# Kernel optimization log

Hardware: AMD Instinct MI355X
Metric: run time of the kernel (lower is better)

The kernel has to match this reference:

```python
import jax, jax.numpy as jnp
import numpy as np

L, H, E, V = 8, 16, 1024, 32000   # n_layer, n_head, n_embd, vocab_size
B, T = 4, 1024                      # batch, block_size
HS = E // H                         # head_size = 64


def _ln(x, g, b, eps=1e-5):
    m = jnp.mean(x, axis=-1, keepdims=True)
    v = jnp.mean((x - m) ** 2, axis=-1, keepdims=True)
    return (x - m) / jnp.sqrt(v + eps) * g + b


def setup_inputs() -> dict:
    key = jax.random.key(0)
    ks = jax.random.split(key, 21)
    s = 0.02
    n = lambda k, shp: (jax.random.normal(k, shp, dtype=jnp.float32) * s)
    return {
        'idx': jax.random.randint(ks[0], (B, T), 0, V),
        'tok_emb': n(ks[1], (V, E)),
        'pos_emb': n(ks[2], (T, E)),
        'ln1_g': jnp.ones((L, E), jnp.float32),
        'ln1_b': jnp.zeros((L, E), jnp.float32),
        'Wq': n(ks[3], (L, E, E)),
        'Wk': n(ks[4], (L, E, E)),
        'Wv': n(ks[5], (L, E, E)),
        'Wo': n(ks[6], (L, E, E)),
        'bo': jnp.zeros((L, E), jnp.float32),
        'ln2_g': jnp.ones((L, E), jnp.float32),
        'ln2_b': jnp.zeros((L, E), jnp.float32),
        'W1': n(ks[7], (L, E, 4 * E)),
        'b1': jnp.zeros((L, 4 * E), jnp.float32),
        'W2': n(ks[8], (L, 4 * E, E)),
        'b2': jnp.zeros((L, E), jnp.float32),
        'lnf_g': jnp.ones((E,), jnp.float32),
        'lnf_b': jnp.zeros((E,), jnp.float32),
        'Wlm': n(ks[9], (E, V)),
        'blm': jnp.zeros((V,), jnp.float32),
    }


def reference(idx, tok_emb, pos_emb, ln1_g, ln1_b, Wq, Wk, Wv, Wo, bo,
              ln2_g, ln2_b, W1, b1, W2, b2, lnf_g, lnf_b, Wlm, blm):
    x = tok_emb[idx] + pos_emb[:T]               # [B, T, E]
    scale = E ** -0.5                            # NOTE: source scales by C=n_embd, not head_size
    mask = jnp.tril(jnp.ones((T, T), dtype=bool))
    for l in range(L):
        h = _ln(x, ln1_g[l], ln1_b[l])
        q = (h @ Wq[l]).reshape(B, T, H, HS).transpose(0, 2, 1, 3)   # [B,H,T,hs]
        k = (h @ Wk[l]).reshape(B, T, H, HS).transpose(0, 2, 1, 3)
        v = (h @ Wv[l]).reshape(B, T, H, HS).transpose(0, 2, 1, 3)
        att = jnp.einsum('bhqd,bhkd->bhqk', q, k) * scale
        att = jnp.where(mask, att, -jnp.inf)
        att = jax.nn.softmax(att, axis=-1)
        o = jnp.einsum('bhqk,bhkd->bhqd', att, v)
        o = o.transpose(0, 2, 1, 3).reshape(B, T, E)                 # concat heads
        x = x + o @ Wo[l] + bo[l]
        h2 = _ln(x, ln2_g[l], ln2_b[l])
        x = x + jax.nn.relu(h2 @ W1[l] + b1[l]) @ W2[l] + b2[l]
    x = _ln(x, lnf_g, lnf_b)
    return x @ Wlm + blm                          # logits [B, T, V]
```

## Files before the change

kernel.cpp:

```cpp
#include <hip/hip_runtime.h>
#include <math.h>

#define L_ 8
#define H_ 16
#define E_ 1024
#define V_ 32000
#define B_ 4
#define T_ 1024
#define HS_ 64
#define M_ 4096
#define QKVS_ 3072

typedef __attribute__((ext_vector_type(8))) short short8;
typedef __attribute__((ext_vector_type(4))) float f32x4;

__device__ __forceinline__ unsigned short f2bf(float f) {
  unsigned int u = __builtin_bit_cast(unsigned int, f);
  u += 0x7fffu + ((u >> 16) & 1u);
  return (unsigned short)(u >> 16);
}
__device__ __forceinline__ float bf2f(unsigned short u) {
  unsigned int v = ((unsigned int)u) << 16;
  return __builtin_bit_cast(float, v);
}

__global__ __launch_bounds__(256) void k_embed(
    const int* __restrict__ idx, const float* __restrict__ tok,
    const float* __restrict__ pos, float* __restrict__ x) {
  int bt = blockIdx.x;
  int t  = bt & (T_ - 1);
  int token = idx[bt];
  const float4* te = (const float4*)(tok + (size_t)token * E_);
  const float4* pe = (const float4*)(pos + (size_t)t * E_);
  float4* xo = (float4*)(x + (size_t)bt * E_);
  int i = threadIdx.x;
  float4 a = te[i], b = pe[i];
  xo[i] = make_float4(a.x + b.x, a.y + b.y, a.z + b.z, a.w + b.w);
}

__global__ __launch_bounds__(256) void k_wt(
    const float* __restrict__ W, unsigned short* __restrict__ WT,
    int K, int N, size_t ss, size_t ds) {
  __shared__ unsigned short t[64][66];
  const float* Ws = W + (size_t)blockIdx.z * ss;
  unsigned short* Wd = WT + (size_t)blockIdx.z * ds;
  int n0 = blockIdx.x * 64, k0 = blockIdx.y * 64;
  int tid = threadIdx.x;
  int c = tid & 63, r4 = tid >> 6;
  #pragma unroll
  for (int i = 0; i < 16; ++i) {
    int kr = i * 4 + r4;
    t[kr][c] = f2bf(Ws[(size_t)(k0 + kr) * N + n0 + c]);
  }
  __syncthreads();
  #pragma unroll
  for (int i = 0; i < 16; ++i) {
    int nr = i * 4 + r4;
    Wd[(size_t)(n0 + nr) * K + k0 + c] = t[c][nr];
  }
}

__device__ __forceinline__ float blk_sum256(float v, float* red) {
  #pragma unroll
  for (int o = 1; o < 64; o <<= 1) v += __shfl_xor(v, o);
  int wid = threadIdx.x >> 6, lane = threadIdx.x & 63;
  if (lane == 0) red[wid] = v;
  __syncthreads();
  v = red[0] + red[1] + red[2] + red[3];
  __syncthreads();
  return v;
}

__global__ __launch_bounds__(256) void k_ln_bf(
    const float* __restrict__ X, const float* __restrict__ g,
    const float* __restrict__ b, unsigned short* __restrict__ Y) {
  __shared__ float red[4];
  int row = blockIdx.x;
  int i = threadIdx.x;
  float4 xv = ((const float4*)(X + (size_t)row * E_))[i];
  float s = xv.x + xv.y + xv.z + xv.w;
  s = blk_sum256(s, red);
  float mean = s * (1.0f / E_);
  float dx = xv.x - mean, dy = xv.y - mean, dz = xv.z - mean, dw = xv.w - mean;
  float vs = dx*dx + dy*dy + dz*dz + dw*dw;
  vs = blk_sum256(vs, red);
  float rstd = rsqrtf(vs * (1.0f / E_) + 1e-5f);
  float4 gv = ((const float4*)g)[i];
  float4 bv = ((const float4*)b)[i];
  ushort4 o;
  o.x = f2bf(dx * rstd * gv.x + bv.x);
  o.y = f2bf(dy * rstd * gv.y + bv.y);
  o.z = f2bf(dz * rstd * gv.z + bv.z);
  o.w = f2bf(dw * rstd * gv.w + bv.w);
  ((ushort4*)(Y + (size_t)row * E_))[i] = o;
}

__global__ __launch_bounds__(256) void k_red4ln(
    const unsigned short* __restrict__ p, const float* __restrict__ bias,
    float* __restrict__ xf, const float* __restrict__ g,
    const float* __restrict__ b, unsigned short* __restrict__ hb) {
  __shared__ float red[4];
  const int ME = M_ * E_;
  int row = blockIdx.x;
  int tid = threadIdx.x;
  int i = row * E_ + tid * 4;
  ushort4 a  = *(const ushort4*)(p + i);
  ushort4 b2 = *(const ushort4*)(p + ME + i);
  ushort4 c  = *(const ushort4*)(p + 2 * ME + i);
  ushort4 d  = *(const ushort4*)(p + 3 * ME + i);
  float4 bv = *(const float4*)(bias + tid * 4);
  float4 x  = *(float4*)(xf + i);
  x.x += bf2f(a.x) + bf2f(b2.x) + bf2f(c.x) + bf2f(d.x) + bv.x;
  x.y += bf2f(a.y) + bf2f(b2.y) + bf2f(c.y) + bf2f(d.y) + bv.y;
  x.z += bf2f(a.z) + bf2f(b2.z) + bf2f(c.z) + bf2f(d.z) + bv.z;
  x.w += bf2f(a.w) + bf2f(b2.w) + bf2f(c.w) + bf2f(d.w) + bv.w;
  *(float4*)(xf + i) = x;
  float s = x.x + x.y + x.z + x.w;
  s = blk_sum256(s, red);
  float mean = s * (1.0f / E_);
  float dx = x.x - mean, dy = x.y - mean, dz = x.z - mean, dw = x.w - mean;
  float vs = dx*dx + dy*dy + dz*dz + dw*dw;
  vs = blk_sum256(vs, red);
  float rstd = rsqrtf(vs * (1.0f / E_) + 1e-5f);
  float4 gv = ((const float4*)g)[tid];
  float4 lb = ((const float4*)b)[tid];
  ushort4 o;
  o.x = f2bf(dx * rstd * gv.x + lb.x);
  o.y = f2bf(dy * rstd * gv.y + lb.y);
  o.z = f2bf(dz * rstd * gv.z + lb.z);
  o.w = f2bf(dw * rstd * gv.w + lb.w);
  ((ushort4*)(hb + (size_t)row * E_))[tid] = o;
}

#define GLDS(src, dst) __builtin_amdgcn_global_load_lds( \
    (const __attribute__((address_space(1))) void*)(src), \
    (__attribute__((address_space(3))) void*)(dst), 16, 0, 0)

#define BAR() do { asm volatile("" ::: "memory"); __builtin_amdgcn_s_barrier(); \
                   asm volatile("" ::: "memory"); } while (0)

template<int OT, bool RELU, int DEC, int NF>
__global__ __launch_bounds__(512, 2) void k_gemm_256(
    const unsigned short* __restrict__ A, const unsigned short* __restrict__ BT,
    const float* __restrict__ bias, void* __restrict__ Cout, int N, int K, int Kstr) {
  constexpr int BUFA = 16384;
  constexpr int BUFB = NF * 4096;
  constexpr int BN = NF * 64;
  __shared__ __attribute__((aligned(16))) unsigned short As[2 * BUFA];
  __shared__ __attribute__((aligned(16))) unsigned short Bs[2 * BUFB];
  int tid = threadIdx.x;
  int lane = tid & 63, w = tid >> 6;
  int lr = lane & 15, lq = (lane >> 4) & 3;
  int wm = w >> 2, wn = w & 3;

  int nwg = gridDim.x, orig = blockIdx.x;
  int qq = nwg >> 3, rr = nwg & 7;
  int xcd = orig & 7, lid = orig >> 3;
  int wg = (xcd < rr ? xcd * (qq + 1) : rr * (qq + 1) + (xcd - rr) * qq) + lid;
  int m0, n0, kofs = 0;
  size_t cofs = 0;
  if constexpr (DEC == 0) { m0 = (wg & 15) * 256; n0 = (wg >> 4) * BN; }
  else if constexpr (DEC == 1) {
    int nbn = N / BN;
    int msub = wg & 7;
    int rest = wg >> 3;
    int nb = rest % nbn;
    int msup = rest / nbn;
    m0 = (msup * 8 + msub) * 256;
    n0 = nb * BN;
  } else {
    int inner = wg & 63;
    m0 = (inner & 15) * 256; n0 = (inner >> 4) * BN;
    int ks = wg >> 6;
    kofs = ks * K;
    cofs = (size_t)ks * M_ * (size_t)N;
  }

  int srow = w * 8 + (lane >> 3);
  int skoff = ((lane & 7) ^ (lane >> 3)) * 8;
  const unsigned short* aS = A + (size_t)(m0 + srow) * Kstr + kofs + skoff;
  const unsigned short* bS = BT + (size_t)(n0 + srow) * Kstr + kofs + skoff;

#define STG_A1(bo, g, tt) GLDS(aS + (size_t)((g) * 64) * Kstr + (tt) * 64, \
                               &As[(bo) + (((g) * 64) << 6) + (w << 9)])
#define STG_B1(bo, g, tt) GLDS(bS + (size_t)((g) * 64) * Kstr + (tt) * 64, \
                               &Bs[(bo) + (((g) * 64) << 6) + (w << 9)])
#define LDA_(dst, mh, ks) { _Pragma("unroll") for (int m_ = 0; m_ < 4; ++m_) \
  dst[m_] = *(const short8*)&As[soA + ((wm * 128 + (mh) * 64 + m_ * 16 + lr) << 6) + ((((ks) * 4 + lq) ^ (lr & 7)) << 3)]; }
#define LDB_(dst, ks) { _Pragma("unroll") for (int n_ = 0; n_ < NF; ++n_) \
  dst[n_] = *(const short8*)&Bs[soB + ((wn * (16 * NF) + n_ * 16 + lr) << 6) + ((((ks) * 4 + lq) ^ (lr & 7)) << 3)]; }
#define MMA(afr, mofs) do { __builtin_amdgcn_s_setprio(1); \
  _Pragma("unroll") for (int m_ = 0; m_ < 4; ++m_) { \
    _Pragma("unroll") for (int n_ = 0; n_ < NF; ++n_) \
      acc[(mofs) + m_][n_] = __builtin_amdgcn_mfma_f32_16x16x32_bf16(afr[m_], bfr[n_], acc[(mofs) + m_][n_], 0, 0, 0); } \
  __builtin_amdgcn_s_setprio(0); } while (0)

  f32x4 acc[8][NF] = {};
  const int NT = K >> 6;

  #pragma unroll
  for (int g = 0; g < 4; ++g) STG_A1(0, g, 0);
  #pragma unroll
  for (int g = 0; g < NF; ++g) STG_B1(0, g, 0);
  if (NT > 1) {
    STG_B1(BUFB, 0, 1); STG_B1(BUFB, 1, 1);
    asm volatile("s_waitcnt vmcnt(2)" ::: "memory");
  } else {
    asm volatile("s_waitcnt vmcnt(0)" ::: "memory");
  }
  BAR();

  for (int t = 0; t < NT; ++t) {
    const int soA = (t & 1) * BUFA, soB = (t & 1) * BUFB;
    const int nbA = ((t + 1) & 1) * BUFA, nbB = ((t + 1) & 1) * BUFB;
    short8 af0[4], af1[4], bfr[NF];
    LDA_(af0, 0, 0);
    LDB_(bfr, 0);
    if (t + 1 < NT) {
      STG_B1(nbB, 2, t + 1);
      if constexpr (NF == 4) STG_B1(nbB, 3, t + 1);
    }
    BAR(); MMA(af0, 0); BAR();
    LDA_(af1, 1, 0);
    if (t + 1 < NT) { STG_A1(nbA, 0, t + 1); STG_A1(nbA, 1, t + 1); }
    BAR(); MMA(af1, 4); BAR();
    LDA_(af0, 0, 1);
    LDB_(bfr, 1);
    if (t + 1 < NT) { STG_A1(nbA, 2, t + 1); STG_A1(nbA, 3, t + 1); }
    BAR(); MMA(af0, 0); BAR();
    LDA_(af1, 1, 1);
    if (t + 2 < NT) { STG_B1(soB, 0, t + 2); STG_B1(soB, 1, t + 2); }
    BAR(); MMA(af1, 4);
    if (t + 2 < NT) { asm volatile("s_waitcnt vmcnt(2)" ::: "memory"); }
    else            { asm volatile("s_waitcnt vmcnt(0)" ::: "memory"); }
    BAR();
  }

  #pragma unroll
  for (int m = 0; m < 8; ++m) {
    #pragma unroll
    for (int n = 0; n < NF; ++n) {
      int col = n0 + wn * (16 * NF) + n * 16 + lr;
      float bv = bias ? bias[col] : 0.0f;
      #pragma unroll
      for (int i = 0; i < 4; ++i) {
        size_t row = (size_t)(m0 + wm * 128 + m * 16 + lq * 4 + i);
        float v = acc[m][n][i] + bv;
        if (RELU) v = fmaxf(v, 0.0f);
        if (OT == 0) ((float*)Cout)[cofs + row * N + col] = v;
        else ((unsigned short*)Cout)[cofs + row * N + col] = f2bf(v);
      }
    }
  }
#undef STG_A1
#undef STG_B1
#undef LDA_
#undef LDB_
#undef MMA
}

template<int BN, int OT, bool RELU, bool RES>
__global__ __launch_bounds__(256) void k_gemm_tn(
    const unsigned short* __restrict__ A, const unsigned short* __restrict__ BT,
    const float* __restrict__ bias, const float* __restrict__ R,
    void* __restrict__ Cout, int M, int N, int K) {
  constexpr int NF = BN / 32;
  __shared__ __attribute__((aligned(16))) unsigned short As[128 * 64];
  __shared__ __attribute__((aligned(16))) unsigned short Bs[BN * 64];
  int tid = threadIdx.x;
  int lane = tid & 63, w = tid >> 6;
  int lr = lane & 15, lq = lane >> 4;
  int m0 = blockIdx.x * 128, n0 = blockIdx.y * BN;
  int wr = (w >> 1) * 64, wc = (w & 1) * (BN / 2);

  int srow = w * 8 + (lane >> 3);
  int skoff = ((lane & 7) ^ (lane >> 3)) * 8;
  const unsigned short* a0 = A + (size_t)(m0 + srow) * K + skoff;
  const unsigned short* b0 = BT + (size_t)(n0 + srow) * K + skoff;

  f32x4 acc[4][NF] = {};

  for (int k0 = 0; k0 < K; k0 += 64) {
    __syncthreads();
    #pragma unroll
    for (int j = 0; j < 4; ++j)
      __builtin_amdgcn_global_load_lds(
          (const __attribute__((address_space(1))) void*)(a0 + (size_t)(j * 32) * K + k0),
          (__attribute__((address_space(3))) void*)(As + j * 2048 + w * 512), 16, 0, 0);
    #pragma unroll
    for (int j = 0; j < NF; ++j)
      __builtin_amdgcn_global_load_lds(
          (const __attribute__((address_space(1))) void*)(b0 + (size_t)(j * 32) * K + k0),
          (__attribute__((address_space(3))) void*)(Bs + j * 2048 + w * 512), 16, 0, 0);
    __syncthreads();
    short8 af[4][2], bf[NF][2];
    #pragma unroll
    for (int m = 0; m < 4; ++m)
      #pragma unroll
      for (int ks = 0; ks < 2; ++ks)
        af[m][ks] = *(const short8*)&As[(wr + m * 16 + lr) * 64 + (((ks * 4 + lq) ^ (lr & 7)) << 3)];
    #pragma unroll
    for (int n = 0; n < NF; ++n)
      #pragma unroll
      for (int ks = 0; ks < 2; ++ks)
        bf[n][ks] = *(const short8*)&Bs[(wc + n * 16 + lr) * 64 + (((ks * 4 + lq) ^ (lr & 7)) << 3)];
    #pragma unroll
    for (int ks = 0; ks < 2; ++ks)
      #pragma unroll
      for (int m = 0; m < 4; ++m)
        #pragma unroll
        for (int n = 0; n < NF; ++n)
          acc[m][n] = __builtin_amdgcn_mfma_f32_16x16x32_bf16(af[m][ks], bf[n][ks], acc[m][n], 0, 0, 0);
  }

  #pragma unroll
  for (int m = 0; m < 4; ++m) {
    #pragma unroll
    for (int n = 0; n < NF; ++n) {
      int col = n0 + wc + n * 16 + lr;
      float bv = bias ? bias[col] : 0.0f;
      #pragma unroll
      for (int i = 0; i < 4; ++i) {
        size_t row = (size_t)(m0 + wr + m * 16 + lq * 4 + i);
        float v = acc[m][n][i] + bv;
        if (RELU) v = fmaxf(v, 0.0f);
        if (RES)  v += R[row * N + col];
        if (OT == 0) ((float*)Cout)[row * N + col] = v;
        else ((unsigned short*)Cout)[row * N + col] = f2bf(v);
      }
    }
  }
}

template<int OT, bool RELU, bool RES>
__global__ __launch_bounds__(256) void k_gemm_bf(
    const unsigned short* __restrict__ A, const float* __restrict__ W,
    const float* __restrict__ bias, const float* __restrict__ R,
    void* __restrict__ Cout, int M, int N, int K) {
  __shared__ unsigned short As[128][40];
  __shared__ unsigned short Bs[128][40];
  int tid = threadIdx.x;
  int lane = tid & 63, wid = tid >> 6;
  int m0 = blockIdx.x * 128, n0 = blockIdx.y * 128;
  int wr = (wid >> 1) * 64, wc = (wid & 1) * 64;
  f32x4 acc[4][4] = {};
  int a_row = tid >> 1, a_koff = (tid & 1) * 16;
  int b_nb = tid & 31, b_kb = (tid >> 5) * 4;
  int lr = lane & 15, lq = lane >> 4;
  for (int k0 = 0; k0 < K; k0 += 32) {
    const unsigned short* ap = A + (size_t)(m0 + a_row) * K + k0 + a_koff;
    uint4 av0 = *(const uint4*)ap;
    uint4 av1 = *(const uint4*)(ap + 8);
    float wv[4][4];
    #pragma unroll
    for (int dk = 0; dk < 4; ++dk) {
      const float* wrow = W + (size_t)(k0 + b_kb + dk) * N + n0 + b_nb;
      #pragma unroll
      for (int j = 0; j < 4; ++j) wv[j][dk] = wrow[32 * j];
    }
    __syncthreads();
    *(uint4*)&As[a_row][a_koff]     = av0;
    *(uint4*)&As[a_row][a_koff + 8] = av1;
    #pragma unroll
    for (int j = 0; j < 4; ++j) {
      ushort4 pk;
      pk.x = f2bf(wv[j][0]); pk.y = f2bf(wv[j][1]);
      pk.z = f2bf(wv[j][2]); pk.w = f2bf(wv[j][3]);
      *(ushort4*)&Bs[b_nb + 32 * j][b_kb] = pk;
    }
    __syncthreads();
    short8 af[4], bf[4];
    #pragma unroll
    for (int m = 0; m < 4; ++m) af[m] = *(const short8*)&As[wr + m * 16 + lr][lq * 8];
    #pragma unroll
    for (int n = 0; n < 4; ++n) bf[n] = *(const short8*)&Bs[wc + n * 16 + lr][lq * 8];
    #pragma unroll
    for (int m = 0; m < 4; ++m)
      #pragma unroll
      for (int n = 0; n < 4; ++n)
        acc[m][n] = __builtin_amdgcn_mfma_f32_16x16x32_bf16(af[m], bf[n], acc[m][n], 0, 0, 0);
  }
  #pragma unroll
  for (int m = 0; m < 4; ++m) {
    #pragma unroll
    for (int n = 0; n < 4; ++n) {
      int col = n0 + wc + n * 16 + lr;
      float bv = bias ? bias[col] : 0.0f;
      #pragma unroll
      for (int i = 0; i < 4; ++i) {
        size_t row = (size_t)(m0 + wr + m * 16 + lq * 4 + i);
        float v = acc[m][n][i] + bv;
        if (RELU) v = fmaxf(v, 0.0f);
        if (RES)  v += R[row * N + col];
        if (OT == 0) ((float*)Cout)[row * N + col] = v;
        else ((unsigned short*)Cout)[row * N + col] = f2bf(v);
      }
    }
  }
}

__global__ __launch_bounds__(256) void k_fattn(
    const unsigned short* __restrict__ QKV, unsigned short* __restrict__ O) {
  __shared__ unsigned short Ks[64][72];
  __shared__ unsigned short Vs[64][74];
  __shared__ unsigned short Pl[4][32][72];
  int tid = threadIdx.x;
  int lane = tid & 63, wid = tid >> 6;
  int lr = lane & 15, lq = lane >> 4;
  int qt = blockIdx.x, bh = blockIdx.y;
  int b = bh >> 4, h = bh & 15;
  size_t base = ((size_t)b * T_) * QKVS_ + h * HS_;
  int q0w = qt * 128 + wid * 32;

  short8 qf[2][2];
  #pragma unroll
  for (int g = 0; g < 2; ++g)
    #pragma unroll
    for (int s = 0; s < 2; ++s)
      qf[g][s] = *(const short8*)(QKV + base + (size_t)(q0w + g * 16 + lr) * QKVS_ + s * 32 + lq * 8);

  f32x4 o_acc[2][4] = {};
  float mrun[2][4], lrun[2][4];
  #pragma unroll
  for (int g = 0; g < 2; ++g)
    #pragma unroll
    for (int i = 0; i < 4; ++i) { mrun[g][i] = -1e30f; lrun[g][i] = 0.0f; }
  const float sc = 0.03125f * 1.44269504f;
  int r = tid >> 2, cc = (tid & 3) * 16;
  int ntiles = 2 * qt + 2;

  uint4 kA0, kA1, vA0, vA1;
  {
    const unsigned short* kp = QKV + base + 1024 + (size_t)r * QKVS_ + cc;
    kA0 = *(const uint4*)kp; kA1 = *(const uint4*)(kp + 8);
    vA0 = *(const uint4*)(kp + 1024); vA1 = *(const uint4*)(kp + 1032);
  }

  for (int t = 0; t < ntiles; ++t) {
    __syncthreads();
    *(uint4*)&Ks[r][cc] = kA0;
    *(uint4*)&Ks[r][cc + 8] = kA1;
    unsigned short vt[16];
    *(uint4*)&vt[0] = vA0; *(uint4*)&vt[8] = vA1;
    #pragma unroll
    for (int j = 0; j < 16; ++j) Vs[cc + j][r] = vt[j];
    __syncthreads();
    if (t + 1 < ntiles) {
      const unsigned short* kp = QKV + base + 1024 + (size_t)((t + 1) * 64 + r) * QKVS_ + cc;
      kA0 = *(const uint4*)kp; kA1 = *(const uint4*)(kp + 8);
      vA0 = *(const uint4*)(kp + 1024); vA1 = *(const uint4*)(kp + 1032);
    }

    f32x4 sa[2][4] = {};
    #pragma unroll
    for (int nt = 0; nt < 4; ++nt)
      #pragma unroll
      for (int s = 0; s < 2; ++s) {
        short8 kf = *(const short8*)&Ks[nt * 16 + lr][s * 32 + lq * 8];
        sa[0][nt] = __builtin_amdgcn_mfma_f32_16x16x32_bf16(qf[0][s], kf, sa[0][nt], 0, 0, 0);
        sa[1][nt] = __builtin_amdgcn_mfma_f32_16x16x32_bf16(qf[1][s], kf, sa[1][nt], 0, 0, 0);
      }

    bool diag = (t >= 2 * qt);
    float p[2][4][4];
    #pragma unroll
    for (int g = 0; g < 2; ++g)
      #pragma unroll
      for (int nt = 0; nt < 4; ++nt)
        #pragma unroll
        for (int i = 0; i < 4; ++i) {
          float v = sa[g][nt][i] * sc;
          if (diag && (t * 64 + nt * 16 + lr > q0w + g * 16 + lq * 4 + i)) v = -1e30f;
          p[g][nt][i] = v;
        }
    #pragma unroll
    for (int g = 0; g < 2; ++g)
      #pragma unroll
      for (int i = 0; i < 4; ++i) {
        float v = fmaxf(fmaxf(p[g][0][i], p[g][1][i]), fmaxf(p[g][2][i], p[g][3][i]));
        #pragma unroll
        for (int o = 1; o < 16; o <<= 1) v = fmaxf(v, __shfl_xor(v, o));
        if (v > mrun[g][i] + 10.0f) {
          float corr = __builtin_amdgcn_exp2f(mrun[g][i] - v);
          mrun[g][i] = v;
          lrun[g][i] *= corr;
          #pragma unroll
          for (int dn = 0; dn < 4; ++dn) o_acc[g][dn][i] *= corr;
        }
        float mn = mrun[g][i];
        float ps = 0.0f;
        #pragma unroll
        for (int nt = 0; nt < 4; ++nt) {
          float pe = __builtin_amdgcn_exp2f(p[g][nt][i] - mn);
          p[g][nt][i] = pe;
          ps += pe;
        }
        lrun[g][i] += ps;
      }
    #pragma unroll
    for (int g = 0; g < 2; ++g)
      #pragma unroll
      for (int nt = 0; nt < 4; ++nt)
        #pragma unroll
        for (int i = 0; i < 4; ++i)
          Pl[wid][g * 16 + lq * 4 + i][nt * 16 + lr] = f2bf(p[g][nt][i]);

    #pragma unroll
    for (int s = 0; s < 2; ++s) {
      short8 pa0 = *(const short8*)&Pl[wid][lr][s * 32 + lq * 8];
      short8 pa1 = *(const short8*)&Pl[wid][16 + lr][s * 32 + lq * 8];
      #pragma unroll
      for (int dn = 0; dn < 4; ++dn) {
        short8 vf = *(const short8*)&Vs[dn * 16 + lr][s * 32 + lq * 8];
        o_acc[0][dn] = __builtin_amdgcn_mfma_f32_16x16x32_bf16(pa0, vf, o_acc[0][dn], 0, 0, 0);
        o_acc[1][dn] = __builtin_amdgcn_mfma_f32_16x16x32_bf16(pa1, vf, o_acc[1][dn], 0, 0, 0);
      }
    }
  }

  #pragma unroll
  for (int g = 0; g < 2; ++g)
    #pragma unroll
    for (int i = 0; i < 4; ++i) {
      float v = lrun[g][i];
      #pragma unroll
      for (int o = 1; o < 16; o <<= 1) v += __shfl_xor(v, o);
      lrun[g][i] = 1.0f / v;
    }
  #pragma unroll
  for (int g = 0; g < 2; ++g)
    #pragma unroll
    for (int dn = 0; dn < 4; ++dn)
      #pragma unroll
      for (int i = 0; i < 4; ++i) {
        size_t row = (size_t)(b * T_) + q0w + g * 16 + lq * 4 + i;
        O[row * E_ + h * HS_ + dn * 16 + lr] = f2bf(o_acc[g][dn][i] * lrun[g][i]);
      }
}

extern "C" void kernel_launch(void* const* d_in, const int* in_sizes, int n_in,
                              void* d_out, int out_size, void* d_ws, size_t ws_size,
                              hipStream_t stream) {
  const int*   idx  = (const int*)d_in[0];
  const float* tok  = (const float*)d_in[1];
  const float* pos  = (const float*)d_in[2];
  const float* ln1g = (const float*)d_in[3];
  const float* ln1b = (const float*)d_in[4];
  const float* Wq   = (const float*)d_in[5];
  const float* Wk   = (const float*)d_in[6];
  const float* Wv   = (const float*)d_in[7];
  const float* Wo   = (const float*)d_in[8];
  const float* bo   = (const float*)d_in[9];
  const float* ln2g = (const float*)d_in[10];
  const float* ln2b = (const float*)d_in[11];
  const float* W1   = (const float*)d_in[12];
  const float* b1   = (const float*)d_in[13];
  const float* W2   = (const float*)d_in[14];
  const float* b2   = (const float*)d_in[15];
  const float* lnfg = (const float*)d_in[16];
  const float* lnfb = (const float*)d_in[17];
  const float* Wlm  = (const float*)d_in[18];
  const float* blm  = (const float*)d_in[19];

  char* scr = (char*)d_out;
  const size_t MB = 1024 * 1024;
  float*          xf    = (float*)(scr);
  unsigned short* qkvb  = (unsigned short*)(scr + 16 * MB);
  unsigned short* ob    = (unsigned short*)(scr + 40 * MB);
  unsigned short* mh    = (unsigned short*)(scr + 48 * MB);
  unsigned short* wqkvT = (unsigned short*)(scr + 80 * MB);
  unsigned short* woT   = (unsigned short*)(scr + 128 * MB);
  unsigned short* w1T   = (unsigned short*)(scr + 144 * MB);
  unsigned short* w2T   = (unsigned short*)(scr + 208 * MB);
  unsigned short* p2    = (unsigned short*)(scr + 280 * MB);
  unsigned short* hb    = (unsigned short*)d_ws;
  unsigned short* wlmT  = (unsigned short*)((char*)d_ws + 8 * MB);
  const size_t EE = (size_t)E_ * E_;
  bool lm_fast = ws_size >= 8 * MB + (size_t)V_ * E_ * 2 + 1024;

  k_embed<<<M_, 256, 0, stream>>>(idx, tok, pos, xf);

  k_wt<<<dim3(16, 16, L_), 256, 0, stream>>>(Wq, wqkvT,          E_, E_, EE, 3 * EE);
  k_wt<<<dim3(16, 16, L_), 256, 0, stream>>>(Wk, wqkvT + EE,     E_, E_, EE, 3 * EE);
  k_wt<<<dim3(16, 16, L_), 256, 0, stream>>>(Wv, wqkvT + 2 * EE, E_, E_, EE, 3 * EE);
  k_wt<<<dim3(16, 16, L_), 256, 0, stream>>>(Wo, woT,            E_, E_, EE, EE);
  k_wt<<<dim3(64, 16, L_), 256, 0, stream>>>(W1, w1T, E_, 4 * E_, 4 * EE, 4 * EE);
  k_wt<<<dim3(16, 64, L_), 256, 0, stream>>>(W2, w2T, 4 * E_, E_, 4 * EE, 4 * EE);
  if (lm_fast)
    k_wt<<<dim3(V_ / 64, 16, 1), 256, 0, stream>>>(Wlm, wlmT, E_, V_, 0, 0);

  k_ln_bf<<<M_, 256, 0, stream>>>(xf, ln1g, ln1b, hb);

  for (int l = 0; l < L_; ++l) {
    k_gemm_256<1, false, 0, 3><<<16 * (QKVS_ / 192), 512, 0, stream>>>(
        hb, wqkvT + (size_t)l * 3 * EE, nullptr, qkvb, QKVS_, E_, E_);
    k_fattn<<<dim3(T_ / 128, B_ * H_), 256, 0, stream>>>(qkvb, ob);
    k_gemm_tn<64, 0, false, true><<<dim3(32, 16), 256, 0, stream>>>(
        ob, woT + (size_t)l * EE, bo + l * E_, xf, xf, M_, E_, E_);
    k_ln_bf<<<M_, 256, 0, stream>>>(xf, ln2g + l * E_, ln2b + l * E_, hb);
    k_gemm_256<1, true, 0, 4><<<16 * (4 * E_ / 256), 512, 0, stream>>>(
        hb, w1T + (size_t)l * 4 * EE, b1 + (size_t)l * 4 * E_, mh, 4 * E_, E_, E_);
    k_gemm_256<1, false, 2, 4><<<256, 512, 0, stream>>>(
        mh, w2T + (size_t)l * 4 * EE, nullptr, p2, E_, E_, 4 * E_);
    const float* ng = (l + 1 < L_) ? (ln1g + (size_t)(l + 1) * E_) : lnfg;
    const float* nb = (l + 1 < L_) ? (ln1b + (size_t)(l + 1) * E_) : lnfb;
    k_red4ln<<<M_, 256, 0, stream>>>(p2, b2 + l * E_, xf, ng, nb, hb);
  }
  if (lm_fast)
    k_gemm_256<0, false, 1, 4><<<16 * (V_ / 256), 512, 0, stream>>>(
        hb, wlmT, blm, (float*)d_out, V_, E_, E_);
  else
    k_gemm_bf<0, false, false><<<dim3(32, V_ / 128), 256, 0, stream>>>(
        hb, Wlm, blm, nullptr, (float*)d_out, M_, V_, E_);
}
```

Measured before the change: 2.453 ms.

## Add K=32-tile LM-head GEMM with smaller LDS for higher occupancy; vectorize weight transpose

Measured after the change: 4.526 ms. 1.84x slower.

```diff
diff --git a/kernel.cpp b/kernel.cpp
--- a/kernel.cpp
+++ b/kernel.cpp
@@ -41,22 +41,28 @@
 __global__ __launch_bounds__(256) void k_wt(
     const float* __restrict__ W, unsigned short* __restrict__ WT,
     int K, int N, size_t ss, size_t ds) {
-  __shared__ unsigned short t[64][66];
+  __shared__ unsigned short t[64][68];
   const float* Ws = W + (size_t)blockIdx.z * ss;
   unsigned short* Wd = WT + (size_t)blockIdx.z * ds;
   int n0 = blockIdx.x * 64, k0 = blockIdx.y * 64;
   int tid = threadIdx.x;
-  int c = tid & 63, r4 = tid >> 6;
-  #pragma unroll
-  for (int i = 0; i < 16; ++i) {
-    int kr = i * 4 + r4;
-    t[kr][c] = f2bf(Ws[(size_t)(k0 + kr) * N + n0 + c]);
+  int c4 = (tid & 15) * 4, r16 = tid >> 4;
+  #pragma unroll
+  for (int i = 0; i < 4; ++i) {
+    int kr = i * 16 + r16;
+    float4 v = *(const float4*)&Ws[(size_t)(k0 + kr) * N + n0 + c4];
+    ushort4 pk;
+    pk.x = f2bf(v.x); pk.y = f2bf(v.y); pk.z = f2bf(v.z); pk.w = f2bf(v.w);
+    *(ushort4*)&t[kr][c4] = pk;
   }
   __syncthreads();
   #pragma unroll
-  for (int i = 0; i < 16; ++i) {
-    int nr = i * 4 + r4;
-    Wd[(size_t)(n0 + nr) * K + k0 + c] = t[c][nr];
+  for (int i = 0; i < 4; ++i) {
+    int nr = i * 16 + r16;
+    ushort4 o;
+    o.x = t[c4 + 0][nr]; o.y = t[c4 + 1][nr];
+    o.z = t[c4 + 2][nr]; o.w = t[c4 + 3][nr];
+    *(ushort4*)&Wd[(size_t)(n0 + nr) * K + k0 + c4] = o;
   }
 }
 
@@ -160,15 +166,7 @@
   int m0, n0, kofs = 0;
   size_t cofs = 0;
   if constexpr (DEC == 0) { m0 = (wg & 15) * 256; n0 = (wg >> 4) * BN; }
-  else if constexpr (DEC == 1) {
-    int nbn = N / BN;
-    int msub = wg & 7;
-    int rest = wg >> 3;
-    int nb = rest % nbn;
-    int msup = rest / nbn;
-    m0 = (msup * 8 + msub) * 256;
-    n0 = nb * BN;
-  } else {
+  else {
     int inner = wg & 63;
     m0 = (inner & 15) * 256; n0 = (inner >> 4) * BN;
     int ks = wg >> 6;
@@ -257,6 +255,96 @@
 #undef LDA_
 #undef LDB_
 #undef MMA
+}
+
+__global__ __launch_bounds__(512, 4) void k_gemm_k32(
+    const unsigned short* __restrict__ A, const unsigned short* __restrict__ BT,
+    const float* __restrict__ bias, float* __restrict__ Cout, int N, int K) {
+  constexpr int BUF = 8192;
+  __shared__ __attribute__((aligned(16))) unsigned short As[2 * BUF];
+  __shared__ __attribute__((aligned(16))) unsigned short Bs[2 * BUF];
+  int tid = threadIdx.x;
+  int lane = tid & 63, w = tid >> 6;
+  int lr = lane & 15, lq = (lane >> 4) & 3;
+  int wm = w >> 2, wn = w & 3;
+
+  int nwg = gridDim.x, orig = blockIdx.x;
+  int qq = nwg >> 3, rr = nwg & 7;
+  int xcd = orig & 7, lid = orig >> 3;
+  int wg = (xcd < rr ? xcd * (qq + 1) : rr * (qq + 1) + (xcd - rr) * qq) + lid;
+  int nbn = N >> 8;
+  int msub = wg & 7;
+  int rest = wg >> 3;
+  int nb = rest % nbn;
+  int msup = rest / nbn;
+  int m0 = (msup * 8 + msub) * 256;
+  int n0 = nb * 256;
+
+  int srow = w * 16 + (lane >> 2);
+  int skoff = ((lane & 3) ^ ((lane >> 2) & 3)) * 8;
+  const unsigned short* aS = A + (size_t)(m0 + srow) * K + skoff;
+  const unsigned short* bS = BT + (size_t)(n0 + srow) * K + skoff;
+
+#define STG32_A(bo, u, tt) GLDS(aS + (size_t)((u) * 128) * K + (tt) * 32, \
+                                &As[(bo) + (u) * 4096 + (w << 9)])
+#define STG32_B(bo, u, tt) GLDS(bS + (size_t)((u) * 128) * K + (tt) * 32, \
+                                &Bs[(bo) + (u) * 4096 + (w << 9)])
+#define LDA32_(dst, mh) { _Pragma("unroll") for (int m_ = 0; m_ < 4; ++m_) \
+  dst[m_] = *(const short8*)&As[so + ((wm * 128 + (mh) * 64 + m_ * 16 + lr) << 5) + ((lq ^ (lr & 3)) << 3)]; }
+#define LDB32_(dst) { _Pragma("unroll") for (int n_ = 0; n_ < 4; ++n_) \
+  dst[n_] = *(const short8*)&Bs[so + ((wn * 64 + n_ * 16 + lr) << 5) + ((lq ^ (lr & 3)) << 3)]; }
+#define MMA32(afr, mofs) do { __builtin_amdgcn_s_setprio(1); \
+  _Pragma("unroll") for (int m_ = 0; m_ < 4; ++m_) { \
+    _Pragma("unroll") for (int n_ = 0; n_ < 4; ++n_) \
+      acc[(mofs) + m_][n_] = __builtin_amdgcn_mfma_f32_16x16x32_bf16(afr[m_], bfr[n_], acc[(mofs) + m_][n_], 0, 0, 0); } \
+  __builtin_amdgcn_s_setprio(0); } while (0)
+
+  f32x4 acc[8][4] = {};
+  const int NT = K >> 5;
+
+  STG32_A(0, 0, 0); STG32_A(0, 1, 0); STG32_B(0, 0, 0); STG32_B(0, 1, 0);
+  if (NT > 1) {
+    STG32_B(BUF, 0, 1); STG32_B(BUF, 1, 1);
+    asm volatile("s_waitcnt vmcnt(2)" ::: "memory");
+  } else {
+    asm volatile("s_waitcnt vmcnt(0)" ::: "memory");
+  }
+  BAR();
+
+  for (int t = 0; t < NT; ++t) {
+    const int so = (t & 1) * BUF;
+    const int nbuf = ((t + 1) & 1) * BUF;
+    short8 af0[4], af1[4], bfr[4];
+    LDA32_(af0, 0);
+    LDB32_(bfr);
+    if (t + 1 < NT) { STG32_A(nbuf, 0, t + 1); STG32_A(nbuf, 1, t + 1); }
+    BAR(); MMA32(af0, 0); BAR();
+    LDA32_(af1, 1);
+    if (t + 2 < NT) { STG32_B(so, 0, t + 2); STG32_B(so, 1, t + 2); }
+    BAR(); MMA32(af1, 4);
+    if (t + 2 < NT) { asm volatile("s_waitcnt vmcnt(2)" ::: "memory"); }
+    else            { asm volatile("s_waitcnt vmcnt(0)" ::: "memory"); }
+    BAR();
+  }
+
+  #pragma unroll
+  for (int m = 0; m < 8; ++m) {
+    #pragma unroll
+    for (int n = 0; n < 4; ++n) {
+      int col = n0 + wn * 64 + n * 16 + lr;
+      float bv = bias ? bias[col] : 0.0f;
+      #pragma unroll
+      for (int i = 0; i < 4; ++i) {
+        size_t row = (size_t)(m0 + wm * 128 + m * 16 + lq * 4 + i);
+        Cout[row * N + col] = acc[m][n][i] + bv;
+      }
+    }
+  }
+#undef STG32_A
+#undef STG32_B
+#undef LDA32_
+#undef LDB32_
+#undef MMA32
 }
 
 template<int BN, int OT, bool RELU, bool RES>
@@ -607,8 +695,8 @@
     k_red4ln<<<M_, 256, 0, stream>>>(p2, b2 + l * E_, xf, ng, nb, hb);
   }
   if (lm_fast)
-    k_gemm_256<0, false, 1, 4><<<16 * (V_ / 256), 512, 0, stream>>>(
-        hb, wlmT, blm, (float*)d_out, V_, E_, E_);
+    k_gemm_k32<<<16 * (V_ / 256), 512, 0, stream>>>(
+        hb, wlmT, blm, (float*)d_out, V_, E_);
   else
     k_gemm_bf<0, false, false><<<dim3(32, V_ / 128), 256, 0, stream>>>(
         hb, Wlm, blm, nullptr, (float*)d_out, M_, V_, E_);
```
